# Performance work log

Hardware: AMD Instinct MI355X
Metric: run time of the kernel (lower is better)

## Reference

```python
import jax, jax.numpy as jnp
import numpy as np

B, C, L = 32, 8, 2048
K, S = 512, 64  # num_shapelets, shapelets_size


def setup_inputs() -> dict:
    key = jax.random.key(0)
    k1, k2 = jax.random.split(key)
    x = jax.random.normal(k1, (B, C, L), dtype=jnp.float32)
    shapelets = jax.random.normal(k2, (C, K, S), dtype=jnp.float32)
    return {"x": x, "shapelets": shapelets}


def reference(x, shapelets):
    # x: [B, C, L]; shapelets: [C, K, S]
    s = shapelets.shape[-1]
    n_dims = x.shape[1]
    W = x.shape[2] - s + 1  # number of sliding windows
    # unfold(2, S, 1): gather overlapping windows -> [B, C, W, S]
    idx = jnp.arange(W)[:, None] + jnp.arange(s)[None, :]
    xw = x[:, :, idx]
    # L2-normalize windows along window length (clamp min like torch)
    xw = xw / jnp.maximum(jnp.linalg.norm(xw, axis=-1, keepdims=True), 1e-8)
    # L2-normalize shapelets along length
    sn = shapelets / jnp.maximum(jnp.linalg.norm(shapelets, axis=-1, keepdims=True), 1e-8)
    # matmul [B,C,W,S] @ [C,S,K] then sum over C, fused into one einsum -> [B, W, K]
    sim = jnp.einsum('bcws,cks->bwk', xw, sn) / n_dims
    sim = jax.nn.relu(sim)
    # max over window positions -> [B, K]; keep the singleton channel dim like torch ([B,1,K])
    out = jnp.max(sim, axis=1)
    return out[:, None, :]
```

## Files before the change

### kernel.cpp

```cpp
#include <hip/hip_runtime.h>


#define B_ 32
#define C_ 8
#define L_ 2048
#define K_ 512
#define S_ 64
#define W_ 1985
#define TW 64

typedef _Float16 f16x8 __attribute__((ext_vector_type(8)));
typedef float f32x16 __attribute__((ext_vector_type(16)));
typedef float f32x4u __attribute__((ext_vector_type(4), aligned(4)));

__global__ __launch_bounds__(256)
void prep_k(const float* __restrict__ x, const float* __restrict__ sh,
            _Float16* __restrict__ Bp, float* __restrict__ invn,
            float* __restrict__ out) {
    __shared__ float xr[L_];
    const int tid = threadIdx.x;
    const int blk = blockIdx.x;

    if (blk < 128) {
        const int sb   = blk * 4 + (tid >> 6);
        const int c    = sb >> 6;
        const int kq   = (sb >> 4) & 3;
        const int nt   = sb & 15;
        const int lane = tid & 63;
        const int n    = lane & 31;
        const int half = lane >> 5;
        const int q    = nt * 32 + n;

        const float4* sp = (const float4*)(sh + (size_t)(c * K_ + q) * S_);
        float ss = 0.f;
        #pragma unroll
        for (int i = 0; i < 8; ++i) {
            float4 v = sp[half * 8 + i];
            ss += v.x * v.x + v.y * v.y + v.z * v.z + v.w * v.w;
        }
        ss += __shfl_xor(ss, 32);
        float inv = 1.f / fmaxf(sqrtf(ss), 1e-8f);

        float4 u0 = sp[kq * 4 + half * 2];
        float4 u1 = sp[kq * 4 + half * 2 + 1];
        f16x8 o;
        o[0] = (_Float16)(u0.x * inv); o[1] = (_Float16)(u0.y * inv);
        o[2] = (_Float16)(u0.z * inv); o[3] = (_Float16)(u0.w * inv);
        o[4] = (_Float16)(u1.x * inv); o[5] = (_Float16)(u1.y * inv);
        o[6] = (_Float16)(u1.z * inv); o[7] = (_Float16)(u1.w * inv);
        ((f16x8*)Bp)[((c * 4 + kq) * 16 + nt) * 64 + lane] = o;
    } else {
        const int r = blk - 128;
        const float* xp = x + (size_t)r * L_;
        for (int i = tid; i < L_ / 4; i += 256)
            ((float4*)xr)[i] = ((const float4*)xp)[i];
        __syncthreads();

        float* ivp = invn + (size_t)r * L_;
        const int w0 = tid * 8;
        float ss = 0.f;
        if (w0 < W_) {
            #pragma unroll
            for (int j = 0; j < S_; ++j) { float v = xr[w0 + j]; ss += v * v; }
        }
        #pragma unroll
        for (int u = 0; u < 8; ++u) {
            int w = w0 + u;
            float o = 0.f;
            if (u > 0 && w < W_)
                ss += xr[w + 63] * xr[w + 63] - xr[w - 1] * xr[w - 1];
            if (w < W_) o = 0.125f / fmaxf(sqrtf(ss), 1e-8f);
            if (w < L_) ivp[w] = o;
        }
        if (r < 64) out[r * 256 + tid] = 0.f;
    }
}

__global__ __launch_bounds__(256, 3)
void mcs_k(const float* __restrict__ x, const _Float16* __restrict__ Bp,
           const float* __restrict__ invn, float* __restrict__ out) {
    __shared__ float invs[C_ * TW];
    __shared__ f16x8 Ah[2][16 * 64];

    const int wt  = blockIdx.x;
    const int ng  = blockIdx.y;
    const int b   = blockIdx.z;
    const int w0  = wt * TW;
    const int tid = threadIdx.x;
    const int lane = tid & 63;
    const int wv   = tid >> 6;

    for (int i = tid; i < C_ * TW; i += 256) {
        int c = i >> 6, w = i & 63;
        invs[i] = invn[(size_t)(b * C_ + c) * L_ + w0 + w];
    }

    auto build = [&](int cp, int buf) {
        const int c0 = cp * 2;
        #pragma unroll
        for (int it = 0; it < 4; ++it) {
            int i  = tid + it * 256;
            int f  = i >> 6, l = i & 63;
            int ch = f >> 3, mt = (f >> 2) & 1, ks = f & 3;
            int m  = mt * 32 + (l & 31);
            int p  = w0 + m + ks * 16 + (l >> 5) * 8;
            int pc = p <= L_ - 8 ? p : L_ - 8;
            const float* xrow = x + (size_t)(b * C_ + c0 + ch) * L_;
            f32x4u v0 = *(const f32x4u*)(xrow + pc);
            f32x4u v1 = *(const f32x4u*)(xrow + pc + 4);
            float iv = invs[(c0 + ch) * TW + m];
            f16x8 o;
            o[0] = (_Float16)(v0[0] * iv); o[1] = (_Float16)(v0[1] * iv);
            o[2] = (_Float16)(v0[2] * iv); o[3] = (_Float16)(v0[3] * iv);
            o[4] = (_Float16)(v1[0] * iv); o[5] = (_Float16)(v1[1] * iv);
            o[6] = (_Float16)(v1[2] * iv); o[7] = (_Float16)(v1[3] * iv);
            Ah[buf][f * 64 + l] = o;
        }
    };

    __syncthreads();
    build(0, 0);
    __syncthreads();

    f32x16 acc[2][2];
    #pragma unroll
    for (int mt = 0; mt < 2; ++mt)
        #pragma unroll
        for (int nt = 0; nt < 2; ++nt)
            #pragma unroll
            for (int r = 0; r < 16; ++r) acc[mt][nt][r] = 0.f;

    #pragma unroll 1
    for (int cp = 0; cp < 4; ++cp) {
        const int buf = cp & 1;
        if (cp + 1 < 4) build(cp + 1, buf ^ 1);

        #pragma unroll
        for (int ch = 0; ch < 2; ++ch) {
            const int c = cp * 2 + ch;
            #pragma unroll
            for (int ks = 0; ks < 4; ++ks) {
                f16x8 af[2], bf[2];
                #pragma unroll
                for (int mt = 0; mt < 2; ++mt)
                    af[mt] = Ah[buf][(ch * 8 + mt * 4 + ks) * 64 + lane];
                const f16x8* bpp = (const f16x8*)Bp +
                    ((c * 4 + ks) * 16 + ng * 8 + wv * 2) * 64 + lane;
                #pragma unroll
                for (int nt = 0; nt < 2; ++nt) bf[nt] = bpp[nt * 64];
                #pragma unroll
                for (int nt = 0; nt < 2; ++nt)
                    #pragma unroll
                    for (int mt = 0; mt < 2; ++mt)
                        acc[mt][nt] = __builtin_amdgcn_mfma_f32_32x32x16_f16(
                            af[mt], bf[nt], acc[mt][nt], 0, 0, 0);
            }
        }
        __syncthreads();
    }

    #pragma unroll
    for (int nt = 0; nt < 2; ++nt) {
        float m = 0.f;
        #pragma unroll
        for (int mt = 0; mt < 2; ++mt)
            #pragma unroll
            for (int r = 0; r < 16; ++r)
                m = fmaxf(m, acc[mt][nt][r]);
        m = fmaxf(m, __shfl_xor(m, 32));
        if (lane < 32)
            atomicMax((unsigned int*)(out + b * K_ + ng * 256 + wv * 64 + nt * 32 + lane),
                      __float_as_uint(m));
    }
}

extern "C" void kernel_launch(void* const* d_in, const int* in_sizes, int n_in,
                              void* d_out, int out_size, void* d_ws, size_t ws_size,
                              hipStream_t stream) {
    const float* x  = (const float*)d_in[0];
    const float* sh = (const float*)d_in[1];
    float* out = (float*)d_out;
    _Float16* Bp  = (_Float16*)d_ws;
    float* invn   = (float*)((char*)d_ws + (size_t)K_ * 512 * sizeof(_Float16));

    prep_k<<<dim3(384), dim3(256), 0, stream>>>(x, sh, Bp, invn, out);
    mcs_k<<<dim3(32, 2, B_), dim3(256), 0, stream>>>(x, Bp, invn, out);
}
```

Baseline: 100.7 us.

## Fuse window norm into GEMM kernel and retile to 128 windows by 128 shapelets

Moves the per-window inverse-norm computation out of the prep kernel and into the main MFMA kernel, so the invn workspace round trip goes away. The tile changes from 64 windows x 256 shapelets to 128 windows x 128 shapelets, with waves split 2x2 across M and N. The main loop now handles one channel per iteration, with B fragments prefetched into registers before the next A tile is built. The prep kernel shrinks to shapelet normalization plus output zeroing, and the main kernel's occupancy target drops from 3 to 2 blocks per SM, which means more registers per thread but fewer resident waves.

```diff
diff --git a/kernel.cpp b/kernel.cpp
--- a/kernel.cpp
+++ b/kernel.cpp
@@ -7,78 +7,51 @@
 #define K_ 512
 #define S_ 64
 #define W_ 1985
-#define TW 64
+#define TW 128
 
 typedef _Float16 f16x8 __attribute__((ext_vector_type(8)));
 typedef float f32x16 __attribute__((ext_vector_type(16)));
 typedef float f32x4u __attribute__((ext_vector_type(4), aligned(4)));
 
 __global__ __launch_bounds__(256)
-void prep_k(const float* __restrict__ x, const float* __restrict__ sh,
-            _Float16* __restrict__ Bp, float* __restrict__ invn,
+void prep_k(const float* __restrict__ sh, _Float16* __restrict__ Bp,
             float* __restrict__ out) {
-    __shared__ float xr[L_];
     const int tid = threadIdx.x;
     const int blk = blockIdx.x;
+    int gid = blk * 256 + tid;
+    if (gid < B_ * K_) out[gid] = 0.f;
 
-    if (blk < 128) {
-        const int sb   = blk * 4 + (tid >> 6);
-        const int c    = sb >> 6;
-        const int kq   = (sb >> 4) & 3;
-        const int nt   = sb & 15;
-        const int lane = tid & 63;
-        const int n    = lane & 31;
-        const int half = lane >> 5;
-        const int q    = nt * 32 + n;
+    const int sb   = blk * 4 + (tid >> 6);
+    const int c    = sb >> 6;
+    const int kq   = (sb >> 4) & 3;
+    const int nt   = sb & 15;
+    const int lane = tid & 63;
+    const int half = lane >> 5;
+    const int q    = nt * 32 + (lane & 31);
 
-        const float4* sp = (const float4*)(sh + (size_t)(c * K_ + q) * S_);
-        float ss = 0.f;
-        #pragma unroll
-        for (int i = 0; i < 8; ++i) {
-            float4 v = sp[half * 8 + i];
-            ss += v.x * v.x + v.y * v.y + v.z * v.z + v.w * v.w;
-        }
-        ss += __shfl_xor(ss, 32);
-        float inv = 1.f / fmaxf(sqrtf(ss), 1e-8f);
+    const float4* sp = (const float4*)(sh + (size_t)(c * K_ + q) * S_);
+    float ss = 0.f;
+    #pragma unroll
+    for (int i = 0; i < 8; ++i) {
+        float4 v = sp[half * 8 + i];
+        ss += v.x * v.x + v.y * v.y + v.z * v.z + v.w * v.w;
+    }
+    ss += __shfl_xor(ss, 32);
+    float inv = 1.f / fmaxf(sqrtf(ss), 1e-8f);
 
-        float4 u0 = sp[kq * 4 + half * 2];
-        float4 u1 = sp[kq * 4 + half * 2 + 1];
-        f16x8 o;
-        o[0] = (_Float16)(u0.x * inv); o[1] = (_Float16)(u0.y * inv);
-        o[2] = (_Float16)(u0.z * inv); o[3] = (_Float16)(u0.w * inv);
-        o[4] = (_Float16)(u1.x * inv); o[5] = (_Float16)(u1.y * inv);
-        o[6] = (_Float16)(u1.z * inv); o[7] = (_Float16)(u1.w * inv);
-        ((f16x8*)Bp)[((c * 4 + kq) * 16 + nt) * 64 + lane] = o;
-    } else {
-        const int r = blk - 128;
-        const float* xp = x + (size_t)r * L_;
-        for (int i = tid; i < L_ / 4; i += 256)
-            ((float4*)xr)[i] = ((const float4*)xp)[i];
-        __syncthreads();
-
-        float* ivp = invn + (size_t)r * L_;
-        const int w0 = tid * 8;
-        float ss = 0.f;
-        if (w0 < W_) {
-            #pragma unroll
-            for (int j = 0; j < S_; ++j) { float v = xr[w0 + j]; ss += v * v; }
-        }
-        #pragma unroll
-        for (int u = 0; u < 8; ++u) {
-            int w = w0 + u;
-            float o = 0.f;
-            if (u > 0 && w < W_)
-                ss += xr[w + 63] * xr[w + 63] - xr[w - 1] * xr[w - 1];
-            if (w < W_) o = 0.125f / fmaxf(sqrtf(ss), 1e-8f);
-            if (w < L_) ivp[w] = o;
-        }
-        if (r < 64) out[r * 256 + tid] = 0.f;
-    }
+    float4 u0 = sp[kq * 4 + half * 2];
+    float4 u1 = sp[kq * 4 + half * 2 + 1];
+    f16x8 o;
+    o[0] = (_Float16)(u0.x * inv); o[1] = (_Float16)(u0.y * inv);
+    o[2] = (_Float16)(u0.z * inv); o[3] = (_Float16)(u0.w * inv);
+    o[4] = (_Float16)(u1.x * inv); o[5] = (_Float16)(u1.y * inv);
+    o[6] = (_Float16)(u1.z * inv); o[7] = (_Float16)(u1.w * inv);
+    ((f16x8*)Bp)[((c * 4 + kq) * 16 + nt) * 64 + lane] = o;
 }
 
-__global__ __launch_bounds__(256, 3)
+__global__ __launch_bounds__(256, 2)
 void mcs_k(const float* __restrict__ x, const _Float16* __restrict__ Bp,
-           const float* __restrict__ invn, float* __restrict__ out) {
+           float* __restrict__ out) {
     __shared__ float invs[C_ * TW];
     __shared__ f16x8 Ah[2][16 * 64];
 
@@ -89,32 +62,52 @@
     const int tid = threadIdx.x;
     const int lane = tid & 63;
     const int wv   = tid >> 6;
+    const int mg   = wv >> 1;
+    const int nw   = wv & 1;
 
-    for (int i = tid; i < C_ * TW; i += 256) {
-        int c = i >> 6, w = i & 63;
-        invs[i] = invn[(size_t)(b * C_ + c) * L_ + w0 + w];
+    {
+        const int c  = tid >> 5;
+        const int g  = tid & 31;
+        const int wb = w0 + g * 4;
+        const float* xr = x + (size_t)(b * C_ + c) * L_;
+        float ss = 0.f;
+        #pragma unroll
+        for (int j = 0; j < S_; ++j) {
+            int idx = wb + j;
+            float v = idx < L_ ? xr[idx] : 0.f;
+            ss += v * v;
+        }
+        #pragma unroll
+        for (int u = 0; u < 4; ++u) {
+            int w = wb + u;
+            invs[c * TW + g * 4 + u] =
+                (w < W_) ? 0.125f / fmaxf(sqrtf(ss), 1e-8f) : 0.f;
+            float pv = xr[w];
+            int ni = w + S_;
+            float nv = ni < L_ ? xr[ni] : 0.f;
+            ss += nv * nv - pv * pv;
+        }
     }
 
-    auto build = [&](int cp, int buf) {
-        const int c0 = cp * 2;
+    auto build = [&](int cN, int bufN) {
+        const float* xrow = x + (size_t)(b * C_ + cN) * L_;
         #pragma unroll
         for (int it = 0; it < 4; ++it) {
             int i  = tid + it * 256;
             int f  = i >> 6, l = i & 63;
-            int ch = f >> 3, mt = (f >> 2) & 1, ks = f & 3;
-            int m  = mt * 32 + (l & 31);
+            int mgb = f >> 3, mt = (f >> 2) & 1, ks = f & 3;
+            int m  = mgb * 64 + mt * 32 + (l & 31);
             int p  = w0 + m + ks * 16 + (l >> 5) * 8;
             int pc = p <= L_ - 8 ? p : L_ - 8;
-            const float* xrow = x + (size_t)(b * C_ + c0 + ch) * L_;
             f32x4u v0 = *(const f32x4u*)(xrow + pc);
             f32x4u v1 = *(const f32x4u*)(xrow + pc + 4);
-            float iv = invs[(c0 + ch) * TW + m];
+            float iv = invs[cN * TW + m];
             f16x8 o;
             o[0] = (_Float16)(v0[0] * iv); o[1] = (_Float16)(v0[1] * iv);
             o[2] = (_Float16)(v0[2] * iv); o[3] = (_Float16)(v0[3] * iv);
             o[4] = (_Float16)(v1[0] * iv); o[5] = (_Float16)(v1[1] * iv);
             o[6] = (_Float16)(v1[2] * iv); o[7] = (_Float16)(v1[3] * iv);
-            Ah[buf][f * 64 + l] = o;
+            Ah[bufN][f * 64 + l] = o;
         }
     };
 
@@ -131,30 +124,33 @@
             for (int r = 0; r < 16; ++r) acc[mt][nt][r] = 0.f;
 
     #pragma unroll 1
-    for (int cp = 0; cp < 4; ++cp) {
-        const int buf = cp & 1;
-        if (cp + 1 < 4) build(cp + 1, buf ^ 1);
+    for (int c = 0; c < C_; ++c) {
+        const int buf = c & 1;
+
+        f16x8 bfr[4][2];
+        {
+            const f16x8* bbase = (const f16x8*)Bp +
+                ((c * 4) * 16 + ng * 4 + nw * 2) * 64 + lane;
+            #pragma unroll
+            for (int ks = 0; ks < 4; ++ks)
+                #pragma unroll
+                for (int nt = 0; nt < 2; ++nt)
+                    bfr[ks][nt] = bbase[(ks * 16 + nt) * 64];
+        }
+
+        if (c + 1 < C_) build(c + 1, buf ^ 1);
 
         #pragma unroll
-        for (int ch = 0; ch < 2; ++ch) {
-            const int c = cp * 2 + ch;
+        for (int ks = 0; ks < 4; ++ks) {
+            f16x8 af[2];
+            af[0] = Ah[buf][(mg * 8 + ks) * 64 + lane];
+            af[1] = Ah[buf][(mg * 8 + 4 + ks) * 64 + lane];
             #pragma unroll
-            for (int ks = 0; ks < 4; ++ks) {
-                f16x8 af[2], bf[2];
+            for (int nt = 0; nt < 2; ++nt)
                 #pragma unroll
                 for (int mt = 0; mt < 2; ++mt)
-                    af[mt] = Ah[buf][(ch * 8 + mt * 4 + ks) * 64 + lane];
-                const f16x8* bpp = (const f16x8*)Bp +
-                    ((c * 4 + ks) * 16 + ng * 8 + wv * 2) * 64 + lane;
-                #pragma unroll
-                for (int nt = 0; nt < 2; ++nt) bf[nt] = bpp[nt * 64];
-                #pragma unroll
-                for (int nt = 0; nt < 2; ++nt)
-                    #pragma unroll
-                    for (int mt = 0; mt < 2; ++mt)
-                        acc[mt][nt] = __builtin_amdgcn_mfma_f32_32x32x16_f16(
-                            af[mt], bf[nt], acc[mt][nt], 0, 0, 0);
-            }
+                    acc[mt][nt] = __builtin_amdgcn_mfma_f32_32x32x16_f16(
+                        af[mt], bfr[ks][nt], acc[mt][nt], 0, 0, 0);
         }
         __syncthreads();
     }
@@ -169,7 +165,7 @@
                 m = fmaxf(m, acc[mt][nt][r]);
         m = fmaxf(m, __shfl_xor(m, 32));
         if (lane < 32)
-            atomicMax((unsigned int*)(out + b * K_ + ng * 256 + wv * 64 + nt * 32 + lane),
+            atomicMax((unsigned int*)(out + b * K_ + ng * 128 + nw * 64 + nt * 32 + lane),
                       __float_as_uint(m));
     }
 }
@@ -181,8 +177,7 @@
     const float* sh = (const float*)d_in[1];
     float* out = (float*)d_out;
     _Float16* Bp  = (_Float16*)d_ws;
-    float* invn   = (float*)((char*)d_ws + (size_t)K_ * 512 * sizeof(_Float16));
 
-    prep_k<<<dim3(384), dim3(256), 0, stream>>>(x, sh, Bp, invn, out);
-    mcs_k<<<dim3(32, 2, B_), dim3(256), 0, stream>>>(x, Bp, invn, out);
+    prep_k<<<dim3(128), dim3(256), 0, stream>>>(sh, Bp, out);
+    mcs_k<<<dim3(16, 4, B_), dim3(256), 0, stream>>>(x, Bp, out);
 }
```

Result: slower. 129.1 us (+28.1%).

## Build A fragments in registers and enlarge per-wave tile, dropping LDS staging

Applied to the files above, without the earlier changes.

Each wave now loads its x windows straight from global memory into registers, normalizes them and converts to f16, instead of staging them through double-buffered shared memory with block barriers. The window tile grows to 128 and each wave computes a 64x128 output tile (2x4 MFMA accumulators), so B fragments are reused across more rows and half as many blocks launch. The aim is to remove LDS traffic and synchronization and to improve reuse. In exchange register pressure rises (launch bounds drop to 2 blocks per CU), overlapping windows are loaded redundantly from global/L2, and there are fewer blocks (1024) to fill the GPU.

```diff
diff --git a/kernel.cpp b/kernel.cpp
--- a/kernel.cpp
+++ b/kernel.cpp
@@ -7,7 +7,7 @@
 #define K_ 512
 #define S_ 64
 #define W_ 1985
-#define TW 64
+#define TW 128
 
 typedef _Float16 f16x8 __attribute__((ext_vector_type(8)));
 typedef float f32x16 __attribute__((ext_vector_type(16)));
@@ -27,9 +27,8 @@
         const int kq   = (sb >> 4) & 3;
         const int nt   = sb & 15;
         const int lane = tid & 63;
-        const int n    = lane & 31;
         const int half = lane >> 5;
-        const int q    = nt * 32 + n;
+        const int q    = nt * 32 + (lane & 31);
 
         const float4* sp = (const float4*)(sh + (size_t)(c * K_ + q) * S_);
         float ss = 0.f;
@@ -76,91 +75,79 @@
     }
 }
 
-__global__ __launch_bounds__(256, 3)
+__global__ __launch_bounds__(256, 2)
 void mcs_k(const float* __restrict__ x, const _Float16* __restrict__ Bp,
            const float* __restrict__ invn, float* __restrict__ out) {
-    __shared__ float invs[C_ * TW];
-    __shared__ f16x8 Ah[2][16 * 64];
-
     const int wt  = blockIdx.x;
     const int ng  = blockIdx.y;
     const int b   = blockIdx.z;
-    const int w0  = wt * TW;
     const int tid = threadIdx.x;
     const int lane = tid & 63;
     const int wv   = tid >> 6;
+    const int mg   = wv >> 1;
+    const int nw   = wv & 1;
 
-    for (int i = tid; i < C_ * TW; i += 256) {
-        int c = i >> 6, w = i & 63;
-        invs[i] = invn[(size_t)(b * C_ + c) * L_ + w0 + w];
-    }
+    const int l31 = lane & 31;
+    const int lh  = lane >> 5;
+    const int Wb  = wt * TW + mg * 64;
+    const int m0  = Wb + l31;
+    const int m1  = Wb + 32 + l31;
 
-    auto build = [&](int cp, int buf) {
-        const int c0 = cp * 2;
-        #pragma unroll
-        for (int it = 0; it < 4; ++it) {
-            int i  = tid + it * 256;
-            int f  = i >> 6, l = i & 63;
-            int ch = f >> 3, mt = (f >> 2) & 1, ks = f & 3;
-            int m  = mt * 32 + (l & 31);
-            int p  = w0 + m + ks * 16 + (l >> 5) * 8;
-            int pc = p <= L_ - 8 ? p : L_ - 8;
-            const float* xrow = x + (size_t)(b * C_ + c0 + ch) * L_;
-            f32x4u v0 = *(const f32x4u*)(xrow + pc);
-            f32x4u v1 = *(const f32x4u*)(xrow + pc + 4);
-            float iv = invs[(c0 + ch) * TW + m];
-            f16x8 o;
-            o[0] = (_Float16)(v0[0] * iv); o[1] = (_Float16)(v0[1] * iv);
-            o[2] = (_Float16)(v0[2] * iv); o[3] = (_Float16)(v0[3] * iv);
-            o[4] = (_Float16)(v1[0] * iv); o[5] = (_Float16)(v1[1] * iv);
-            o[6] = (_Float16)(v1[2] * iv); o[7] = (_Float16)(v1[3] * iv);
-            Ah[buf][f * 64 + l] = o;
-        }
-    };
-
-    __syncthreads();
-    build(0, 0);
-    __syncthreads();
-
-    f32x16 acc[2][2];
+    f32x16 acc[2][4];
     #pragma unroll
     for (int mt = 0; mt < 2; ++mt)
         #pragma unroll
-        for (int nt = 0; nt < 2; ++nt)
+        for (int nt = 0; nt < 4; ++nt)
             #pragma unroll
             for (int r = 0; r < 16; ++r) acc[mt][nt][r] = 0.f;
 
     #pragma unroll 1
-    for (int cp = 0; cp < 4; ++cp) {
-        const int buf = cp & 1;
-        if (cp + 1 < 4) build(cp + 1, buf ^ 1);
+    for (int c = 0; c < C_; ++c) {
+        const float* ivp  = invn + (size_t)(b * C_ + c) * L_;
+        const float* xrow = x + (size_t)(b * C_ + c) * L_;
+        float iv0 = ivp[m0];
+        float iv1 = ivp[m1];
+
+        const f16x8* bbase = (const f16x8*)Bp +
+            ((c * 4) * 16 + ng * 8 + nw * 4) * 64 + lane;
+        f16x8 bfr[4][4];
+        #pragma unroll
+        for (int ks = 0; ks < 4; ++ks)
+            #pragma unroll
+            for (int nt = 0; nt < 4; ++nt)
+                bfr[ks][nt] = bbase[(ks * 16 + nt) * 64];
+
+        f16x8 af[2][4];
+        #pragma unroll
+        for (int mt = 0; mt < 2; ++mt) {
+            float iv = mt ? iv1 : iv0;
+            #pragma unroll
+            for (int ks = 0; ks < 4; ++ks) {
+                int p  = Wb + mt * 32 + l31 + ks * 16 + lh * 8;
+                int pc = p <= L_ - 8 ? p : L_ - 8;
+                f32x4u v0 = *(const f32x4u*)(xrow + pc);
+                f32x4u v1 = *(const f32x4u*)(xrow + pc + 4);
+                f16x8 o;
+                o[0] = (_Float16)(v0[0] * iv); o[1] = (_Float16)(v0[1] * iv);
+                o[2] = (_Float16)(v0[2] * iv); o[3] = (_Float16)(v0[3] * iv);
+                o[4] = (_Float16)(v1[0] * iv); o[5] = (_Float16)(v1[1] * iv);
+                o[6] = (_Float16)(v1[2] * iv); o[7] = (_Float16)(v1[3] * iv);
+                af[mt][ks] = o;
+            }
+        }
 
         #pragma unroll
-        for (int ch = 0; ch < 2; ++ch) {
-            const int c = cp * 2 + ch;
+        for (int ks = 0; ks < 4; ++ks)
             #pragma unroll
-            for (int ks = 0; ks < 4; ++ks) {
-                f16x8 af[2], bf[2];
+            for (int nt = 0; nt < 4; ++nt)
                 #pragma unroll
                 for (int mt = 0; mt < 2; ++mt)
-                    af[mt] = Ah[buf][(ch * 8 + mt * 4 + ks) * 64 + lane];
-                const f16x8* bpp = (const f16x8*)Bp +
-                    ((c * 4 + ks) * 16 + ng * 8 + wv * 2) * 64 + lane;
-                #pragma unroll
-                for (int nt = 0; nt < 2; ++nt) bf[nt] = bpp[nt * 64];
-                #pragma unroll
-                for (int nt = 0; nt < 2; ++nt)
-                    #pragma unroll
-                    for (int mt = 0; mt < 2; ++mt)
-                        acc[mt][nt] = __builtin_amdgcn_mfma_f32_32x32x16_f16(
-                            af[mt], bf[nt], acc[mt][nt], 0, 0, 0);
-            }
-        }
-        __syncthreads();
+                    acc[mt][nt] = __builtin_amdgcn_mfma_f32_32x32x16_f16(
+                        af[mt][ks], bfr[ks][nt], acc[mt][nt], 0, 0, 0);
     }
 
     #pragma unroll
-    for (int nt = 0; nt < 2; ++nt) {
+    for (int nt = 0; nt < 4; ++nt) {
         float m = 0.f;
         #pragma unroll
         for (int mt = 0; mt < 2; ++mt)
@@ -169,7 +156,7 @@
                 m = fmaxf(m, acc[mt][nt][r]);
         m = fmaxf(m, __shfl_xor(m, 32));
         if (lane < 32)
-            atomicMax((unsigned int*)(out + b * K_ + ng * 256 + wv * 64 + nt * 32 + lane),
+            atomicMax((unsigned int*)(out + b * K_ + ng * 256 + nw * 128 + nt * 32 + l31),
                       __float_as_uint(m));
     }
 }
@@ -184,5 +171,5 @@
     float* invn   = (float*)((char*)d_ws + (size_t)K_ * 512 * sizeof(_Float16));
 
     prep_k<<<dim3(384), dim3(256), 0, stream>>>(x, sh, Bp, invn, out);
-    mcs_k<<<dim3(32, 2, B_), dim3(256), 0, stream>>>(x, Bp, invn, out);
+    mcs_k<<<dim3(16, 2, B_), dim3(256), 0, stream>>>(x, Bp, invn, out);
 }
```

Result: no change. 99.53 us (-1.2%).
